# Performance work log

Measured on AMD Instinct MI355X. Metric: run time of the kernel, lower is better.

Reference implementation:

```python
import jax, jax.numpy as jnp
import numpy as np

IN_CH = 512
HID = 512
SCALE = 1.0 / np.sqrt(16.0)  # hard-coded 16**0.5 in source, not sqrt(hidden)


def setup_inputs() -> dict:
    key = jax.random.key(0)
    ks = jax.random.split(key, 9)
    B, T = 8, 2048
    lim = 1.0 / np.sqrt(IN_CH)
    return {
        "q": jax.random.normal(ks[0], (B, T, IN_CH), dtype=jnp.float32),
        "k": jax.random.normal(ks[1], (B, T, IN_CH), dtype=jnp.float32),
        "v": jax.random.normal(ks[2], (B, T, IN_CH), dtype=jnp.float32),
        "Wq": jax.random.uniform(ks[3], (IN_CH, HID), jnp.float32, -lim, lim),
        "bq": jax.random.uniform(ks[4], (HID,), jnp.float32, -lim, lim),
        "Wk": jax.random.uniform(ks[5], (IN_CH, HID), jnp.float32, -lim, lim),
        "bk": jax.random.uniform(ks[6], (HID,), jnp.float32, -lim, lim),
        "Wv": jax.random.uniform(ks[7], (IN_CH, HID), jnp.float32, -lim, lim),
        "bv": jax.random.uniform(ks[8], (HID,), jnp.float32, -lim, lim),
    }


def reference(q, k, v, Wq, bq, Wk, bk, Wv, bv):
    # Linear projections: [B,T,F] @ [F,H] + [H]
    query = jnp.einsum("btf,fh->bth", q, Wq) + bq
    key_p = jnp.einsum("btf,fh->bth", k, Wk) + bk
    value = jnp.einsum("btf,fh->bth", v, Wv) + bv
    # energy: [B,T,T], scaled by fixed 1/sqrt(16)
    energy = jnp.einsum("bth,bsh->bts", query, key_p) * SCALE
    attn = jax.nn.softmax(energy, axis=-1)
    # weighted sum: [B,T,H]
    return jnp.einsum("bts,bsh->bth", attn, value)
```

## Files before the change

kernel.cpp:

```cpp
#include <hip/hip_runtime.h>
#include <stdint.h>

typedef __bf16 bf16;
typedef bf16 bf16x8 __attribute__((ext_vector_type(8)));
typedef float f32x4 __attribute__((ext_vector_type(4)));

#define MFMA(a, b, c) __builtin_amdgcn_mfma_f32_16x16x32_bf16(a, b, c, 0, 0, 0)

#define SCALE_L2E 0.3606737602222409f
#define M0 16.0f

#define WAITVM(N) asm volatile("s_waitcnt vmcnt(" #N ")" ::: "memory")
#define WAITLGKM0 asm volatile("s_waitcnt lgkmcnt(0)" ::: "memory")
#define SBAR __builtin_amdgcn_s_barrier()
#define SCHEDB __builtin_amdgcn_sched_barrier(0)
#define PRIO(x) __builtin_amdgcn_s_setprio(x)

__device__ __forceinline__ void gload_lds16(const void* g, void* l) {
  __builtin_amdgcn_global_load_lds(
      (const __attribute__((address_space(1))) uint32_t*)g,
      (__attribute__((address_space(3))) uint32_t*)l, 16, 0, 0);
}

__global__ void k_wtrans(const float* __restrict__ Wq, const float* __restrict__ Wk,
                         const float* __restrict__ Wv, bf16* __restrict__ Wt) {
  __shared__ float tile[32][33];
  int x = threadIdx.x, y = threadIdx.y;
  int k0 = blockIdx.x * 32, n0 = blockIdx.y * 32, z = blockIdx.z;
  const float* W = (z == 0) ? Wq : (z == 1) ? Wk : Wv;
  for (int j = 0; j < 4; j++)
    tile[y + 8 * j][x] = W[(size_t)(k0 + y + 8 * j) * 512 + n0 + x];
  __syncthreads();
  bf16* o = Wt + (size_t)z * 262144;
  for (int j = 0; j < 4; j++)
    o[(size_t)(n0 + y + 8 * j) * 512 + k0 + x] = (bf16)tile[x][y + 8 * j];
}

__global__ __launch_bounds__(256, 2) void k_proj(
    const float* __restrict__ q, const float* __restrict__ k, const float* __restrict__ v,
    const bf16* __restrict__ Wt, const float* __restrict__ bq, const float* __restrict__ bk,
    const float* __restrict__ bv, bf16* __restrict__ Qp, bf16* __restrict__ Kp,
    bf16* __restrict__ Vtp) {
  int z = blockIdx.z;
  const float* A = (z == 0) ? q : (z == 1) ? k : v;
  const float* bias = (z == 0) ? bq : (z == 1) ? bk : bv;
  const bf16* Bw = Wt + (size_t)z * 262144;

  int m0 = blockIdx.x * 128, n0 = blockIdx.y * 128;
  __shared__ __align__(16) char smem[65536];
  bf16* As = (bf16*)smem;
  bf16* Bs = (bf16*)(smem + 32768);
  bf16* Ts = (bf16*)smem;

  int tid = threadIdx.x;
  int wave = tid >> 6, lane = tid & 63, qr = lane & 15, quad = lane >> 4;
  int wm = (wave >> 1) * 64, wn = (wave & 1) * 64;

  f32x4 acc[4][4];
  for (int mi = 0; mi < 4; mi++)
    for (int ni = 0; ni < 4; ni++) acc[mi][ni] = (f32x4){0.f, 0.f, 0.f, 0.f};

  float4 rx[4], ry[4];

  auto issue = [&](int kk, int buf) {
#pragma unroll
    for (int i = 0; i < 4; i++) {
      int ch = i * 256 + tid, row = ch >> 3, c = ch & 7;
      const float4* src = (const float4*)(A + (size_t)(m0 + row) * 512 + kk + c * 8);
      rx[i] = src[0];
      ry[i] = src[1];
    }
    SCHEDB;
#pragma unroll
    for (int i = 0; i < 4; i++) {
      int ch = i * 256 + tid, row = ch >> 3, c = ch & 7, cs = c ^ (row & 7);
      gload_lds16(Bw + (size_t)(n0 + row) * 512 + kk + cs * 8, &Bs[buf * 8192 + ch * 8]);
    }
    SCHEDB;
  };

  auto writeA = [&](int buf) {
#pragma unroll
    for (int i = 0; i < 4; i++) {
      int ch = i * 256 + tid, row = ch >> 3, c = ch & 7, cs = c ^ (row & 7);
      bf16x8 t;
      t[0] = (bf16)rx[i].x; t[1] = (bf16)rx[i].y; t[2] = (bf16)rx[i].z; t[3] = (bf16)rx[i].w;
      t[4] = (bf16)ry[i].x; t[5] = (bf16)ry[i].y; t[6] = (bf16)ry[i].z; t[7] = (bf16)ry[i].w;
      *(bf16x8*)&As[buf * 8192 + row * 64 + cs * 8] = t;
    }
  };

  auto compute = [&](int buf) {
    bf16* Ab = &As[buf * 8192];
    bf16* Bb = &Bs[buf * 8192];
#pragma unroll
    for (int h = 0; h < 2; h++) {
      bf16x8 af[4], bfv[4];
#pragma unroll
      for (int mi = 0; mi < 4; mi++) {
        int rr = wm + mi * 16 + qr;
        int cc = (h * 4 + quad) ^ (rr & 7);
        af[mi] = *(bf16x8*)&Ab[rr * 64 + cc * 8];
      }
#pragma unroll
      for (int ni = 0; ni < 4; ni++) {
        int rr = wn + ni * 16 + qr;
        int cc = (h * 4 + quad) ^ (rr & 7);
        bfv[ni] = *(bf16x8*)&Bb[rr * 64 + cc * 8];
      }
#pragma unroll
      for (int mi = 0; mi < 4; mi++)
#pragma unroll
        for (int ni = 0; ni < 4; ni++) acc[mi][ni] = MFMA(af[mi], bfv[ni], acc[mi][ni]);
    }
  };

  issue(0, 0);
  writeA(0);
  WAITLGKM0;
  SBAR;

  for (int t = 0; t < 8; t++) {
    int cur = t & 1;
    if (t < 7) issue((t + 1) * 64, cur ^ 1);
    if (t < 7) { WAITVM(12); } else { WAITVM(0); }
    SBAR;
    SCHEDB;
    compute(cur);
    if (t < 7) writeA(cur ^ 1);
    WAITLGKM0;
    SBAR;
  }

  if (z == 2) {
    for (int ni = 0; ni < 4; ni++) {
      int hcol = wn + ni * 16 + qr;
      float bz = bias[n0 + hcol];
      for (int mi = 0; mi < 4; mi++) {
        int tl = wm + mi * 16 + quad * 4;
        bf16 tmp[4];
        for (int r = 0; r < 4; r++) tmp[r] = (bf16)(acc[mi][ni][r] + bz);
        *(uint64_t*)&Ts[hcol * 136 + tl] = *(uint64_t*)tmp;
      }
    }
    __syncthreads();
    int bb = m0 >> 11, t0l = m0 & 2047;
    for (int i = 0; i < 8; i++) {
      int ch = i * 256 + tid;
      int row = ch >> 4, c = ch & 15;
      *(bf16x8*)(Vtp + (size_t)(bb * 512 + n0 + row) * 2048 + t0l + c * 8) =
          *(bf16x8*)&Ts[row * 136 + c * 8];
    }
  } else {
    bf16* C = (z == 0) ? Qp : Kp;
    float sc = (z == 0) ? SCALE_L2E : 1.0f;
    for (int ni = 0; ni < 4; ni++) {
      int col = n0 + wn + ni * 16 + qr;
      float bz = bias[col];
      for (int mi = 0; mi < 4; mi++) {
        int rbase = m0 + wm + mi * 16 + quad * 4;
        for (int r = 0; r < 4; r++)
          C[(size_t)(rbase + r) * 512 + col] = (bf16)((acc[mi][ni][r] + bz) * sc);
      }
    }
  }
}

__global__ __launch_bounds__(512, 1) void k_qk(const bf16* __restrict__ Qp,
                                               const bf16* __restrict__ Kp,
                                               bf16* __restrict__ P,
                                               float* __restrict__ Lpart) {
  __shared__ __align__(16) bf16 S[65536];
  int b = blockIdx.z;
  const bf16* A = Qp + (size_t)b * 2048 * 512;
  const bf16* B = Kp + (size_t)b * 2048 * 512;
  bf16* Pb = P + (size_t)b * 2048 * 2048;
  int m0 = blockIdx.x * 256, n0 = blockIdx.y * 256;
  int tid = threadIdx.x;
  int wave = tid >> 6, lane = tid & 63, qr = lane & 15, quad = lane >> 4;
  int wm = wave >> 2, wn = wave & 3;

  f32x4 acc[8][4];
  for (int mi = 0; mi < 8; mi++)
    for (int ni = 0; ni < 4; ni++) acc[mi][ni] = (f32x4){0.f, 0.f, 0.f, 0.f};

  auto stageAj = [&](int t, int s, int j) {
    int kk = t * 64;
    bf16* As_ = S + s * 16384;
    int ch = j * 512 + tid, row = ch >> 3, c = ch & 7, cs = c ^ (row & 7);
    gload_lds16(A + (size_t)(m0 + row) * 512 + kk + cs * 8, As_ + ch * 8);
  };
  auto stage = [&](int t, int s) {
    int kk = t * 64;
    bf16* Bs_ = S + 32768 + s * 16384;
#pragma unroll
    for (int j = 0; j < 4; j++) {
      int ch = j * 512 + tid, row = ch >> 3, c = ch & 7, cs = c ^ (row & 7);
      gload_lds16(B + (size_t)(n0 + row) * 512 + kk + cs * 8, Bs_ + ch * 8);
    }
    stageAj(t, s, 0);
    stageAj(t, s, 2);
    stageAj(t, s, 1);
    stageAj(t, s, 3);
  };

  stage(0, 0);
  stage(1, 1);

  for (int t = 0; t < 8; t++) {
    int cur = t & 1;
    bf16* As_ = S + cur * 16384;
    bf16* Bs_ = S + 32768 + cur * 16384;

    if (t < 7) { WAITVM(10); } else { WAITVM(2); }
    SBAR;
    bf16x8 aF[4][2], bF[4][2];
#pragma unroll
    for (int mi = 0; mi < 4; mi++)
#pragma unroll
      for (int kk = 0; kk < 2; kk++) {
        int row = wm * 128 + mi * 16 + qr;
        aF[mi][kk] = *(bf16x8*)&As_[row * 64 + ((kk * 4 + quad) ^ (row & 7)) * 8];
      }
#pragma unroll
    for (int ni = 0; ni < 4; ni++)
#pragma unroll
      for (int kk = 0; kk < 2; kk++) {
        int row = wn * 64 + ni * 16 + qr;
        bF[ni][kk] = *(bf16x8*)&Bs_[row * 64 + ((kk * 4 + quad) ^ (row & 7)) * 8];
      }
    WAITLGKM0;
    SCHEDB;
    PRIO(1);
#pragma unroll
    for (int kk = 0; kk < 2; kk++)
#pragma unroll
      for (int mi = 0; mi < 4; mi++)
#pragma unroll
        for (int ni = 0; ni < 4; ni++)
          acc[mi][ni] = MFMA(aF[mi][kk], bF[ni][kk], acc[mi][ni]);
    PRIO(0);

    if (t < 7) { WAITVM(8); } else { WAITVM(0); }
    SBAR;
#pragma unroll
    for (int mi = 0; mi < 4; mi++)
#pragma unroll
      for (int kk = 0; kk < 2; kk++) {
        int row = wm * 128 + 64 + mi * 16 + qr;
        aF[mi][kk] = *(bf16x8*)&As_[row * 64 + ((kk * 4 + quad) ^ (row & 7)) * 8];
      }
    WAITLGKM0;
    SBAR;
    if (t < 6) stage(t + 2, cur);
    SCHEDB;
    PRIO(1);
#pragma unroll
    for (int kk = 0; kk < 2; kk++)
#pragma unroll
      for (int mi = 0; mi < 4; mi++)
#pragma unroll
        for (int ni = 0; ni < 4; ni++)
          acc[4 + mi][ni] = MFMA(aF[mi][kk], bF[ni][kk], acc[4 + mi][ni]);
    PRIO(0);
  }

  int slice = blockIdx.y * 4 + wn;
  float* Lp = Lpart + (size_t)slice * 16384 + b * 2048;
#pragma unroll
  for (int mi = 0; mi < 8; mi++) {
    int rowb = m0 + wm * 128 + mi * 16 + quad * 4;
#pragma unroll
    for (int r = 0; r < 4; r++) {
      float s = 0.f;
      bf16* prow = Pb + (size_t)(rowb + r) * 2048 + n0 + wn * 64 + qr;
#pragma unroll
      for (int ni = 0; ni < 4; ni++) {
        float e = exp2f(acc[mi][ni][r] - M0);
        prow[ni * 16] = (bf16)e;
        s += e;
      }
      s += __shfl_xor(s, 1);
      s += __shfl_xor(s, 2);
      s += __shfl_xor(s, 4);
      s += __shfl_xor(s, 8);
      if (qr == 0) Lp[rowb + r] = s;
    }
  }
}

__global__ __launch_bounds__(512, 1) void k_pv(const bf16* __restrict__ P,
                                               const bf16* __restrict__ Vtp,
                                               const float* __restrict__ Lpart,
                                               float* __restrict__ out) {
  __shared__ __align__(16) bf16 S[49152];
  int b = blockIdx.z;
  const bf16* A = P + (size_t)b * 2048 * 2048;
  const bf16* B = Vtp + (size_t)b * 512 * 2048;
  int m0 = blockIdx.x * 256, n0 = blockIdx.y * 128;
  int tid = threadIdx.x;
  int wave = tid >> 6, lane = tid & 63, qr = lane & 15, quad = lane >> 4;
  int wmi = wave >> 1, wni = wave & 1;

  float linv_own = 0.f;
  if (tid < 256) {
    float s = 0.f;
    for (int j = 0; j < 32; j++) s += Lpart[(size_t)j * 16384 + b * 2048 + m0 + tid];
    linv_own = 1.0f / s;
  }

  f32x4 acc[4][4];
  for (int mi = 0; mi < 4; mi++)
    for (int ni = 0; ni < 4; ni++) acc[mi][ni] = (f32x4){0.f, 0.f, 0.f, 0.f};

  auto stage = [&](int t, int s) {
    int kk = t * 64;
    bf16* As_ = S + s * 16384;
    bf16* Bs_ = S + 32768 + s * 8192;
#pragma unroll
    for (int j = 0; j < 4; j++) {
      int ch = j * 512 + tid, row = ch >> 3, c = ch & 7, cs = c ^ (row & 7);
      gload_lds16(A + (size_t)(m0 + row) * 2048 + kk + cs * 8, As_ + ch * 8);
    }
#pragma unroll
    for (int j = 0; j < 2; j++) {
      int ch = j * 512 + tid, row = ch >> 3, c = ch & 7, cs = c ^ (row & 7);
      gload_lds16(B + (size_t)(n0 + row) * 2048 + kk + cs * 8, Bs_ + ch * 8);
    }
  };

  stage(0, 0);
  stage(1, 1);

  for (int t = 0; t < 32; t++) {
    int cur = t & 1;
    bf16* As_ = S + cur * 16384;
    bf16* Bs_ = S + 32768 + cur * 8192;

    if (t < 31) { WAITVM(6); } else { WAITVM(0); }
    SBAR;
    bf16x8 aF[4][2], bF[4][2];
#pragma unroll
    for (int mi = 0; mi < 4; mi++)
#pragma unroll
      for (int kk = 0; kk < 2; kk++) {
        int row = wmi * 64 + mi * 16 + qr;
        aF[mi][kk] = *(bf16x8*)&As_[row * 64 + ((kk * 4 + quad) ^ (row & 7)) * 8];
      }
#pragma unroll
    for (int ni = 0; ni < 4; ni++)
#pragma unroll
      for (int kk = 0; kk < 2; kk++) {
        int row = wni * 64 + ni * 16 + qr;
        bF[ni][kk] = *(bf16x8*)&Bs_[row * 64 + ((kk * 4 + quad) ^ (row & 7)) * 8];
      }
    WAITLGKM0;
    SBAR;
    if (t < 30) stage(t + 2, cur);
    SCHEDB;
    PRIO(1);
#pragma unroll
    for (int kk = 0; kk < 2; kk++)
#pragma unroll
      for (int mi = 0; mi < 4; mi++)
#pragma unroll
        for (int ni = 0; ni < 4; ni++)
          acc[mi][ni] = MFMA(aF[mi][kk], bF[ni][kk], acc[mi][ni]);
    PRIO(0);
  }

  WAITLGKM0;
  SBAR;
  float* Linv_s = (float*)S;
  if (tid < 256) Linv_s[tid] = linv_own;
  SBAR;

#pragma unroll
  for (int mi = 0; mi < 4; mi++) {
    int rowl = wmi * 64 + mi * 16 + quad * 4;
    float linv[4];
    for (int r = 0; r < 4; r++) linv[r] = Linv_s[rowl + r];
#pragma unroll
    for (int ni = 0; ni < 4; ni++) {
      int col = n0 + wni * 64 + ni * 16 + qr;
      float* og = out + (size_t)(b * 2048 + m0 + rowl) * 512 + col;
      for (int r = 0; r < 4; r++) og[(size_t)r * 512] = acc[mi][ni][r] * linv[r];
    }
  }
}

extern "C" void kernel_launch(void* const* d_in, const int* in_sizes, int n_in,
                              void* d_out, int out_size, void* d_ws, size_t ws_size,
                              hipStream_t stream) {
  (void)in_sizes; (void)n_in; (void)out_size; (void)ws_size;
  const float* q  = (const float*)d_in[0];
  const float* k  = (const float*)d_in[1];
  const float* v  = (const float*)d_in[2];
  const float* Wq = (const float*)d_in[3];
  const float* bq = (const float*)d_in[4];
  const float* Wk = (const float*)d_in[5];
  const float* bk = (const float*)d_in[6];
  const float* Wv = (const float*)d_in[7];
  const float* bv = (const float*)d_in[8];
  float* out = (float*)d_out;

  char* ws = (char*)d_ws;
  bf16* Wt     = (bf16*)(ws);
  bf16* Qp     = (bf16*)(ws + 1572864);
  bf16* Kp     = (bf16*)(ws + 18350080);
  bf16* Vtp    = (bf16*)(ws + 35127296);
  bf16* P      = (bf16*)(ws + 51904512);
  float* Lpart = (float*)(ws + 119013376);

  k_wtrans<<<dim3(16, 16, 3), dim3(32, 8, 1), 0, stream>>>(Wq, Wk, Wv, Wt);
  k_proj<<<dim3(128, 4, 3), 256, 0, stream>>>(q, k, v, Wt, bq, bk, bv, Qp, Kp, Vtp);
  k_qk<<<dim3(8, 8, 8), 512, 0, stream>>>(Qp, Kp, P, Lpart);
  k_pv<<<dim3(8, 4, 8), 512, 0, stream>>>(P, Vtp, Lpart, out);
}
```

Measured before the change: 262.3 us.

## Prefetch fp32 A-tiles two iterations ahead with double register sets

The projection GEMM's A-operand global loads, which go to registers and are converted to bf16, are now issued two k-steps ahead using two alternating register sets, while the B-tile LDS loads stay one step ahead. The main loop is unrolled by two so each half uses a fixed buffer and register set. This aims to hide more global-load latency behind MFMA compute, at the cost of 32 extra VGPRs, which may reduce occupancy. The vmcnt wait counts must match the new issue order.

```diff
diff --git a/kernel.cpp b/kernel.cpp
--- a/kernel.cpp
+++ b/kernel.cpp
@@ -60,9 +60,10 @@
   for (int mi = 0; mi < 4; mi++)
     for (int ni = 0; ni < 4; ni++) acc[mi][ni] = (f32x4){0.f, 0.f, 0.f, 0.f};
 
-  float4 rx[4], ry[4];
-
-  auto issue = [&](int kk, int buf) {
+  float4 rxA[4], ryA[4];
+  float4 rxB[4], ryB[4];
+
+  auto issueA = [&](int kk, float4 (&rx)[4], float4 (&ry)[4]) {
 #pragma unroll
     for (int i = 0; i < 4; i++) {
       int ch = i * 256 + tid, row = ch >> 3, c = ch & 7;
@@ -71,6 +72,9 @@
       ry[i] = src[1];
     }
     SCHEDB;
+  };
+
+  auto issueB = [&](int kk, int buf) {
 #pragma unroll
     for (int i = 0; i < 4; i++) {
       int ch = i * 256 + tid, row = ch >> 3, c = ch & 7, cs = c ^ (row & 7);
@@ -79,7 +83,7 @@
     SCHEDB;
   };
 
-  auto writeA = [&](int buf) {
+  auto writeA = [&](int buf, float4 (&rx)[4], float4 (&ry)[4]) {
 #pragma unroll
     for (int i = 0; i < 4; i++) {
       int ch = i * 256 + tid, row = ch >> 3, c = ch & 7, cs = c ^ (row & 7);
@@ -115,19 +119,33 @@
     }
   };
 
-  issue(0, 0);
-  writeA(0);
+  issueA(0, rxA, ryA);
+  issueA(64, rxB, ryB);
+  issueB(0, 0);
+  writeA(0, rxA, ryA);
   WAITLGKM0;
   SBAR;
 
-  for (int t = 0; t < 8; t++) {
-    int cur = t & 1;
-    if (t < 7) issue((t + 1) * 64, cur ^ 1);
-    if (t < 7) { WAITVM(12); } else { WAITVM(0); }
-    SBAR;
-    SCHEDB;
-    compute(cur);
-    if (t < 7) writeA(cur ^ 1);
+#pragma unroll
+  for (int t = 0; t < 8; t += 2) {
+    if (t < 6) issueA((t + 2) * 64, rxA, ryA);
+    issueB((t + 1) * 64, 1);
+    if (t < 6) { WAITVM(12); } else { WAITVM(4); }
+    SBAR;
+    SCHEDB;
+    compute(0);
+    writeA(1, rxB, ryB);
+    WAITLGKM0;
+    SBAR;
+
+    int u = t + 1;
+    if (u < 6) issueA((u + 2) * 64, rxB, ryB);
+    if (u < 7) issueB((u + 1) * 64, 0);
+    if (u < 6) { WAITVM(12); } else { WAITVM(0); }
+    SBAR;
+    SCHEDB;
+    compute(1);
+    if (u < 7) writeA(0, rxA, ryA);
     WAITLGKM0;
     SBAR;
   }
```

Result: slower. 272.4 us (+3.9%).
